# Optimization experiments

Measured on AMD Instinct MI355X. Metric: run time of the kernel, lower is better.

Reference implementation:

```python
import jax, jax.numpy as jnp
import numpy as np

B, LAT, H, N, NL = 16, 64, 128, 256, 3
STATS = 7
IU, JU = np.triu_indices(N, 1)  # P = N*(N-1)/2 upper-triangular pairs


def _ln(x, g, b):
    m = jnp.mean(x, axis=-1, keepdims=True)
    v = jnp.var(x, axis=-1, keepdims=True)
    return (x - m) / jnp.sqrt(v + 1e-5) * g + b


def setup_inputs() -> dict:
    key = jax.random.key(0)
    ks = jax.random.split(key, 16)
    s = 0.02  # xavier-ish small gain per _init_weights
    L = NL - 1
    return {
        "x": jax.random.normal(ks[0], (B, LAT), jnp.float32),
        "stats": jax.random.normal(ks[1], (B, STATS), jnp.float32),
        # input_proj: Linear(LAT+7, 2H) + LN(2H)
        "ip_w": jax.random.normal(ks[2], (LAT + STATS, 2 * H)) * s,
        "ip_b": jnp.zeros((2 * H,)),
        "ip_ln_g": jnp.ones((2 * H,)),
        "ip_ln_b": jnp.zeros((2 * H,)),
        # dim_reduce: Linear(2H, H) + LN(H)
        "dr_w": jax.random.normal(ks[3], (2 * H, H)) * s,
        "dr_b": jnp.zeros((H,)),
        "dr_ln_g": jnp.ones((H,)),
        "dr_ln_b": jnp.zeros((H,)),
        # residual blocks (NL-1 of them), proj is Identity since in==out
        "res_lin1_w": jax.random.normal(ks[4], (L, H, H)) * s,
        "res_lin1_b": jnp.zeros((L, H)),
        "res_lin2_w": jax.random.normal(ks[5], (L, H, H)) * s,
        "res_lin2_b": jnp.zeros((L, H)),
        "res_n1_g": jnp.ones((L, H)),
        "res_n1_b": jnp.zeros((L, H)),
        "res_n2_g": jnp.ones((L, H)),
        "res_n2_b": jnp.zeros((L, H)),
        # attention: Linear(H, 1)
        "attn_w": jax.random.normal(ks[6], (H, 1)) * s,
        "attn_b": jnp.zeros((1,)),
        # edge_mlp: Linear(2H, H) + LN(H) + Linear(H, 2)
        "e1_w": jax.random.normal(ks[7], (2 * H, H)) * s,
        "e1_b": jnp.zeros((H,)),
        "e_ln_g": jnp.ones((H,)),
        "e_ln_b": jnp.zeros((H,)),
        "e2_w": jax.random.normal(ks[8], (H, 2)) * s,
        "e2_b": jnp.zeros((2,)),
        "temperature": jnp.ones((1,)) * 0.5,
    }


def reference(x, stats, ip_w, ip_b, ip_ln_g, ip_ln_b, dr_w, dr_b, dr_ln_g,
              dr_ln_b, res_lin1_w, res_lin1_b, res_lin2_w, res_lin2_b,
              res_n1_g, res_n1_b, res_n2_g, res_n2_b, attn_w, attn_b,
              e1_w, e1_b, e_ln_g, e_ln_b, e2_w, e2_b, temperature):
    # concat latent + stats, broadcast to every node: [B, N, LAT+7]
    z = jnp.concatenate([x, stats], axis=-1)
    z = jnp.broadcast_to(z[:, None, :], (B, N, LAT + STATS))
    # input_proj (dropout is identity in eval)
    h = _ln(jax.nn.relu(z @ ip_w + ip_b), ip_ln_g, ip_ln_b)
    # dim_reduce
    h = _ln(jax.nn.relu(h @ dr_w + dr_b), dr_ln_g, dr_ln_b)
    # residual blocks: h = h + 0.1 * block(h); block(h) = mlp(h) + h
    for l in range(res_lin1_w.shape[0]):
        r = _ln(h, res_n1_g[l], res_n1_b[l])
        r = jax.nn.relu(r @ res_lin1_w[l] + res_lin1_b[l])
        r = _ln(r, res_n2_g[l], res_n2_b[l])
        r = r @ res_lin2_w[l] + res_lin2_b[l]
        h = h + 0.1 * (r + h)
    # simple attention over node axis
    w = jax.nn.softmax(h @ attn_w + attn_b, axis=1)  # [B, N, 1]
    h = h * w
    # batched edge MLP over all i<j pairs: [B, P, 2H]
    edge_in = jnp.concatenate([h[:, IU], h[:, JU]], axis=-1)
    e = _ln(jax.nn.relu(edge_in @ e1_w + e1_b), e_ln_g, e_ln_b)
    logits = e @ e2_w + e2_b  # [B, P, 2]
    # gumbel-softmax (hard, straight-through), fixed key for determinism
    temp = jnp.clip(temperature, 0.1, 2.0)
    u = jax.random.uniform(jax.random.key(42), logits.shape,
                           minval=1e-9, maxval=1.0)
    gumbel = -jnp.log(-jnp.log(u))
    y = jax.nn.softmax((logits + gumbel) / temp, axis=-1)
    y_hard = jax.nn.one_hot(jnp.argmax(y, axis=-1), 2, dtype=y.dtype)
    y = y_hard + y - jax.lax.stop_gradient(y)
    xe = y[..., 0]  # [B, P]
    # scatter into upper triangle, symmetrize
    adj = jnp.zeros((B, N, N), dtype=xe.dtype).at[:, IU, JU].set(xe)
    return adj + jnp.swapaxes(adj, 1, 2)
```

## Files before the change

kernel.cpp:

```cpp
#include <hip/hip_runtime.h>
#include <stdint.h>
#include <math.h>

#define BN 16
#define LATN 64
#define STATSN 7
#define ZN 71
#define HN 128
#define H2N 256
#define NNODE 256
#define NPAIR 32640
#define NQ 522240
#define NT 1024

#define BARRIER() asm volatile("s_waitcnt lgkmcnt(0)\n\ts_barrier" ::: "memory")
#define LGKM0()   asm volatile("s_waitcnt lgkmcnt(0)" ::: "memory")

__device__ __forceinline__ void tf2x32(uint32_t x0, uint32_t x1,
                                       uint32_t& o0, uint32_t& o1) {
    const uint32_t ks0 = 0u, ks1 = 42u, ks2 = 0x1BD11BF0u;
    x0 += ks0; x1 += ks1;
#define TFRND(r) { x0 += x1; x1 = (x1 << (r)) | (x1 >> (32 - (r))); x1 ^= x0; }
    TFRND(13) TFRND(15) TFRND(26) TFRND(6)
    x0 += ks1; x1 += ks2 + 1u;
    TFRND(17) TFRND(29) TFRND(16) TFRND(24)
    x0 += ks2; x1 += ks0 + 2u;
    TFRND(13) TFRND(15) TFRND(26) TFRND(6)
    x0 += ks0; x1 += ks1 + 3u;
    TFRND(17) TFRND(29) TFRND(16) TFRND(24)
    x0 += ks1; x1 += ks2 + 4u;
    TFRND(13) TFRND(15) TFRND(26) TFRND(6)
    x0 += ks2; x1 += ks0 + 5u;
#undef TFRND
    o0 = x0; o1 = x1;
}

__device__ __forceinline__ uint32_t bits_partitionable(uint32_t m) {
    uint32_t o0, o1;
    tf2x32(0u, m, o0, o1);
    return o0 ^ o1;
}

__device__ __forceinline__ float bits_to_u(uint32_t w) {
    float f = __uint_as_float((w >> 9) | 0x3f800000u) - 1.0f;
    const float mn = 1e-9f;
    return fmaxf(mn, f * (1.0f - mn) + mn);
}

template<int CTRL>
__device__ __forceinline__ double dppd(double x) {
    int lo = __double2loint(x), hi = __double2hiint(x);
    lo = __builtin_amdgcn_update_dpp(0, lo, CTRL, 0xF, 0xF, true);
    hi = __builtin_amdgcn_update_dpp(0, hi, CTRL, 0xF, 0xF, true);
    return __hiloint2double(hi, lo);
}
__device__ __forceinline__ double swz16d(double x) {
    int lo = __double2loint(x), hi = __double2hiint(x);
    lo = __builtin_amdgcn_ds_swizzle(lo, 0x401F);
    hi = __builtin_amdgcn_ds_swizzle(hi, 0x401F);
    return __hiloint2double(hi, lo);
}
__device__ __forceinline__ void bfly_pair(double& a, double& q) {
    a += dppd<0xB1>(a);   q += dppd<0xB1>(q);
    a += dppd<0x4E>(a);   q += dppd<0x4E>(q);
    a += dppd<0x141>(a);  q += dppd<0x141>(q);
    a += dppd<0x140>(a);  q += dppd<0x140>(q);
    a += swz16d(a);       q += swz16d(q);
    a += __shfl_xor(a, 32, 64);
    q += __shfl_xor(q, 32, 64);
}

template<int K, int O>
struct WS {
    static constexpr int C    = NT / O;
    static constexpr int KC   = (K + C - 1) / C;
    static constexpr int LOGO = (O == 256) ? 8 : 7;
    float w[KC];
    __device__ __forceinline__ void load(const float* __restrict__ W, int t) {
        const int out = t & (O - 1);
        const int k0 = (t >> LOGO) * KC;
#pragma unroll
        for (int i = 0; i < KC; ++i) {
            const int k = k0 + i;
            w[i] = ((K % C == 0) || k < K) ? W[k * O + out] : 0.0f;
        }
    }
    __device__ __forceinline__ double dot(const double* __restrict__ vin, int t) const {
        const int k0 = (t >> LOGO) * KC;
        double a0 = 0.0, a1 = 0.0;
#pragma unroll
        for (int i = 0; i < KC; i += 2) {
            a0 = fma(vin[k0 + i], (double)w[i], a0);
            if (i + 1 < KC) a1 = fma(vin[k0 + i + 1], (double)w[i + 1], a1);
        }
        return a0 + a1;
    }
    __device__ __forceinline__ double dot_mask127(const double* __restrict__ vin, int t) const {
        const int k0 = (t >> LOGO) * KC;
        double a0 = 0.0, a1 = 0.0;
#pragma unroll
        for (int i = 0; i < KC; i += 2) {
            a0 = fma(vin[(k0 + i) & 127], (double)w[i], a0);
            if (i + 1 < KC) a1 = fma(vin[(k0 + i + 1) & 127], (double)w[i + 1], a1);
        }
        return a0 + a1;
    }
};

template<int NV>
__device__ __forceinline__ void w_stats(const float* v, double& m, double& rs) {
    double a = 0.0, q = 0.0;
#pragma unroll
    for (int i = 0; i < NV; ++i) {
        a += (double)v[i];
        q += (double)v[i] * (double)v[i];
    }
    bfly_pair(a, q);
    constexpr double O = (double)(NV * 64);
    m = a * (1.0 / O);
    const double d = q * (1.0 / O) - m * m + 1e-5;
    double r = (double)rsqrtf((float)d);
    r = r * (1.5 - 0.5 * d * r * r);
    r = r * (1.5 - 0.5 * d * r * r);
    rs = r;
}

#define P_IPB   0
#define P_IPG   256
#define P_IPBB  512
#define P_DRB   768
#define P_DRG   896
#define P_DRBB  1024
#define P_R1B   1152
#define P_N1G   1408
#define P_N1B   1664
#define P_N2G   1920
#define P_N2B   2176
#define P_R2B   2432
#define P_E1B   2688
#define P_EG    2816
#define P_EB    2944
#define P_E2W   3072
#define P_E2B   3328
#define P_SIZE  3332

__global__ __launch_bounds__(NT, 1) void logits_kernel(
    const float* __restrict__ x, const float* __restrict__ st,
    const float* __restrict__ ipw, const float* __restrict__ ipb,
    const float* __restrict__ ipg, const float* __restrict__ ipbb,
    const float* __restrict__ drw, const float* __restrict__ drb,
    const float* __restrict__ drg, const float* __restrict__ drbb,
    const float* __restrict__ r1w, const float* __restrict__ r1b,
    const float* __restrict__ r2w, const float* __restrict__ r2b,
    const float* __restrict__ n1g, const float* __restrict__ n1b,
    const float* __restrict__ n2g, const float* __restrict__ n2b,
    const float* __restrict__ e1w, const float* __restrict__ e1b,
    const float* __restrict__ eg,  const float* __restrict__ eb,
    const float* __restrict__ e2w, const float* __restrict__ e2b,
    float* __restrict__ out_logits)
{
    __shared__ __align__(16) double V0[H2N];
    __shared__ __align__(16) double V1[H2N];
    __shared__ double dpA[NT];
    __shared__ double dpB[NT];
    __shared__ float P[P_SIZE];
    const int t = threadIdx.x;
    const int b = blockIdx.x;
    const int l = t & 63;

    WS<ZN, H2N> w_ip;
    WS<H2N, HN> w_dr;
    WS<HN, HN>  w_r1a, w_r2a, w_r1b, w_r2b;
    WS<H2N, HN> w_e1;

    w_ip.load(ipw, t);
    w_dr.load(drw, t);
    if (t < 256) {
        P[P_IPB + t] = ipb[t];  P[P_IPG + t] = ipg[t];  P[P_IPBB + t] = ipbb[t];
        P[P_R1B + t] = r1b[t];  P[P_N1G + t] = n1g[t];  P[P_N1B + t] = n1b[t];
        P[P_N2G + t] = n2g[t];  P[P_N2B + t] = n2b[t];  P[P_R2B + t] = r2b[t];
        P[P_E2W + t] = e2w[t];
    } else if (t < 384) {
        const int i = t - 256;
        P[P_DRB + i] = drb[i];  P[P_DRG + i] = drg[i];  P[P_DRBB + i] = drbb[i];
        P[P_E1B + i] = e1b[i];  P[P_EG + i] = eg[i];    P[P_EB + i] = eb[i];
    } else if (t < 386) {
        P[P_E2B + (t - 384)] = e2b[t - 384];
    }
    if (t < LATN)      V0[t] = (double)x[b * LATN + t];
    else if (t < ZN)   V0[t] = (double)st[b * STATSN + (t - LATN)];
    else if (t < H2N)  V0[t] = 0.0;
    BARRIER();

    float h0 = 0.0f, h1 = 0.0f;

    dpA[t] = w_ip.dot(V0, t);
    w_r1a.load(r1w, t);
    BARRIER();

    {
        float v[4];
#pragma unroll
        for (int i = 0; i < 4; ++i) {
            const int o = l + 64 * i;
            double ca = 0.0;
#pragma unroll
            for (int cc = 0; cc < 4; ++cc) ca += dpA[o + cc * H2N];
            v[i] = fmaxf((float)ca + P[P_IPB + o], 0.0f);
        }
        double m, rs; w_stats<4>(v, m, rs);
#pragma unroll
        for (int i = 0; i < 4; ++i) {
            const int o = l + 64 * i;
            V1[o] = (double)((float)(((double)v[i] - m) * rs) * P[P_IPG + o] + P[P_IPBB + o]);
        }
    }
    LGKM0();
    dpB[t] = w_dr.dot(V1, t);
    w_r2a.load(r2w, t);
    BARRIER();

    {
        float v[2];
#pragma unroll
        for (int i = 0; i < 2; ++i) {
            const int o = l + 64 * i;
            double ca = 0.0;
#pragma unroll
            for (int cc = 0; cc < 8; ++cc) ca += dpB[o + cc * HN];
            v[i] = fmaxf((float)ca + P[P_DRB + o], 0.0f);
        }
        double m, rs; w_stats<2>(v, m, rs);
        h0 = (float)(((double)v[0] - m) * rs) * P[P_DRG + l] + P[P_DRBB + l];
        h1 = (float)(((double)v[1] - m) * rs) * P[P_DRG + l + 64] + P[P_DRBB + l + 64];
        float hv[2] = {h0, h1};
        double m1, rs1; w_stats<2>(hv, m1, rs1);
        V1[l]      = (double)((float)(((double)h0 - m1) * rs1) * P[P_N1G + l] + P[P_N1B + l]);
        V1[l + 64] = (double)((float)(((double)h1 - m1) * rs1) * P[P_N1G + l + 64] + P[P_N1B + l + 64]);
    }
    LGKM0();
    dpA[t] = w_r1a.dot(V1, t);
    w_r1b.load(r1w + HN * HN, t);
    BARRIER();

    {
        float v[2];
#pragma unroll
        for (int i = 0; i < 2; ++i) {
            const int o = l + 64 * i;
            double ca = 0.0;
#pragma unroll
            for (int cc = 0; cc < 8; ++cc) ca += dpA[o + cc * HN];
            v[i] = fmaxf((float)ca + P[P_R1B + o], 0.0f);
        }
        double m, rs; w_stats<2>(v, m, rs);
        V1[l]      = (double)((float)(((double)v[0] - m) * rs) * P[P_N2G + l] + P[P_N2B + l]);
        V1[l + 64] = (double)((float)(((double)v[1] - m) * rs) * P[P_N2G + l + 64] + P[P_N2B + l + 64]);
    }
    LGKM0();
    dpB[t] = w_r2a.dot(V1, t);
    w_r2b.load(r2w + HN * HN, t);
    BARRIER();

    {
        float r2o[2];
#pragma unroll
        for (int i = 0; i < 2; ++i) {
            const int o = l + 64 * i;
            double ca = 0.0;
#pragma unroll
            for (int cc = 0; cc < 8; ++cc) ca += dpB[o + cc * HN];
            r2o[i] = (float)ca + P[P_R2B + o];
        }
        h0 = h0 + 0.1f * (r2o[0] + h0);
        h1 = h1 + 0.1f * (r2o[1] + h1);
        float hv[2] = {h0, h1};
        double m1, rs1; w_stats<2>(hv, m1, rs1);
        V1[l]      = (double)((float)(((double)h0 - m1) * rs1) * P[P_N1G + HN + l] + P[P_N1B + HN + l]);
        V1[l + 64] = (double)((float)(((double)h1 - m1) * rs1) * P[P_N1G + HN + l + 64] + P[P_N1B + HN + l + 64]);
    }
    LGKM0();
    dpA[t] = w_r1b.dot(V1, t);
    w_e1.load(e1w, t);
    BARRIER();

    {
        float v[2];
#pragma unroll
        for (int i = 0; i < 2; ++i) {
            const int o = l + 64 * i;
            double ca = 0.0;
#pragma unroll
            for (int cc = 0; cc < 8; ++cc) ca += dpA[o + cc * HN];
            v[i] = fmaxf((float)ca + P[P_R1B + HN + o], 0.0f);
        }
        double m, rs; w_stats<2>(v, m, rs);
        V1[l]      = (double)((float)(((double)v[0] - m) * rs) * P[P_N2G + HN + l] + P[P_N2B + HN + l]);
        V1[l + 64] = (double)((float)(((double)v[1] - m) * rs) * P[P_N2G + HN + l + 64] + P[P_N2B + HN + l + 64]);
    }
    LGKM0();
    dpB[t] = w_r2b.dot(V1, t);
    BARRIER();

    {
        float r2o[2];
#pragma unroll
        for (int i = 0; i < 2; ++i) {
            const int o = l + 64 * i;
            double ca = 0.0;
#pragma unroll
            for (int cc = 0; cc < 8; ++cc) ca += dpB[o + cc * HN];
            r2o[i] = (float)ca + P[P_R2B + HN + o];
        }
        h0 = h0 + 0.1f * (r2o[0] + h0);
        h1 = h1 + 0.1f * (r2o[1] + h1);
        V0[l]      = (double)h0;
        V0[l + 64] = (double)h1;
    }
    LGKM0();
    dpA[t] = w_e1.dot_mask127(V0, t) * 0.00390625;
    BARRIER();

    {
        float v[2];
#pragma unroll
        for (int i = 0; i < 2; ++i) {
            const int o = l + 64 * i;
            double ca = 0.0;
#pragma unroll
            for (int cc = 0; cc < 8; ++cc) ca += dpA[o + cc * HN];
            v[i] = fmaxf((float)ca + P[P_E1B + o], 0.0f);
        }
        double m, rs; w_stats<2>(v, m, rs);
        const float eo0 = (float)(((double)v[0] - m) * rs) * P[P_EG + l] + P[P_EB + l];
        const float eo1 = (float)(((double)v[1] - m) * rs) * P[P_EG + l + 64] + P[P_EB + l + 64];
        double p0 = (double)eo0 * (double)P[P_E2W + 2 * l];
        p0 = fma((double)eo1, (double)P[P_E2W + 2 * (l + 64)], p0);
        double p1 = (double)eo0 * (double)P[P_E2W + 2 * l + 1];
        p1 = fma((double)eo1, (double)P[P_E2W + 2 * (l + 64) + 1], p1);
        bfly_pair(p0, p1);
        if (t == 0) {
            out_logits[b * 2]     = (float)p0 + P[P_E2B];
            out_logits[b * 2 + 1] = (float)p1 + P[P_E2B + 1];
        }
    }
}

__device__ __forceinline__ int rowbase(int i) { return (i * (2 * NNODE - 1 - i)) >> 1; }

__global__ __launch_bounds__(256) void edges_kernel(const float* __restrict__ lg,
                                                    const float* __restrict__ tptr,
                                                    float* __restrict__ out)
{
    int q = blockIdx.x * blockDim.x + threadIdx.x;
    if (q >= NQ) return;
    if (q < BN * NNODE) {
        int bb = q >> 8, ii = q & 255;
        out[(bb << 16) | (ii << 8) | ii] = 0.0f;
    }
    float temp = fminf(fmaxf(tptr[0], 0.1f), 2.0f);

    int b = q / NPAIR;
    int p = q - b * NPAIR;
    float discf = 261121.0f - 8.0f * (float)p;
    int i = (int)((511.0f - sqrtf(discf)) * 0.5f);
    if (i < 0) i = 0;
    if (i > NNODE - 2) i = NNODE - 2;
    while (rowbase(i + 1) <= p) ++i;
    while (rowbase(i) > p) --i;
    int j = p - rowbase(i) + i + 1;

    uint32_t w0 = bits_partitionable((uint32_t)(2 * q));
    uint32_t w1 = bits_partitionable((uint32_t)(2 * q + 1));

    float u0 = bits_to_u(w0), u1 = bits_to_u(w1);
    float g0 = -logf(-logf(u0));
    float g1 = -logf(-logf(u1));
    float l0 = lg[2 * b], l1 = lg[2 * b + 1];
    float A0 = (l0 + g0) / temp, A1 = (l1 + g1) / temp;
    float mx = fmaxf(A0, A1);
    float e0 = expf(A0 - mx), e1 = expf(A1 - mx);
    float ssum = e0 + e1;
    float y0 = e0 / ssum, y1 = e1 / ssum;
    float xe = (y0 >= y1) ? 1.0f : 0.0f;
    out[(b << 16) | (i << 8) | j] = xe;
    out[(b << 16) | (j << 8) | i] = xe;
}

extern "C" void kernel_launch(void* const* d_in, const int* in_sizes, int n_in,
                              void* d_out, int out_size, void* d_ws, size_t ws_size,
                              hipStream_t stream)
{
    const float* x    = (const float*)d_in[0];
    const float* st   = (const float*)d_in[1];
    const float* ipw  = (const float*)d_in[2];
    const float* ipb  = (const float*)d_in[3];
    const float* ipg  = (const float*)d_in[4];
    const float* ipbb = (const float*)d_in[5];
    const float* drw  = (const float*)d_in[6];
    const float* drb  = (const float*)d_in[7];
    const float* drg  = (const float*)d_in[8];
    const float* drbb = (const float*)d_in[9];
    const float* r1w  = (const float*)d_in[10];
    const float* r1b  = (const float*)d_in[11];
    const float* r2w  = (const float*)d_in[12];
    const float* r2b  = (const float*)d_in[13];
    const float* n1g  = (const float*)d_in[14];
    const float* n1b  = (const float*)d_in[15];
    const float* n2g  = (const float*)d_in[16];
    const float* n2b  = (const float*)d_in[17];
    const float* e1w  = (const float*)d_in[20];
    const float* e1b  = (const float*)d_in[21];
    const float* eg   = (const float*)d_in[22];
    const float* eb   = (const float*)d_in[23];
    const float* e2w  = (const float*)d_in[24];
    const float* e2b  = (const float*)d_in[25];
    const float* temp = (const float*)d_in[26];
    float* out = (float*)d_out;
    float* lg  = (float*)d_ws;

    hipLaunchKernelGGL(logits_kernel, dim3(BN), dim3(NT), 0, stream,
        x, st, ipw, ipb, ipg, ipbb, drw, drb, drg, drbb,
        r1w, r1b, r2w, r2b, n1g, n1b, n2g, n2b,
        e1w, e1b, eg, eb, e2w, e2b, lg);
    hipLaunchKernelGGL(edges_kernel, dim3((NQ + 255) / 256), dim3(256), 0, stream,
        lg, temp, out);
}
```

Measured before the change: 27.33 us.

## Halve block threads and load weights from global inside each dot product

Reduces the per-batch MLP kernel from 1024 to 512 threads, so each thread covers twice as many K elements per output and the cross-thread partial-sum reduction uses half as many slices. The register-prefetched weight structs are removed, and weights are now read directly from global memory inside each matvec rather than being prefetched one stage ahead. This shrinks register pressure and block size, but exposes global load latency on the serial critical path and lengthens each thread's dot-product chain.

```diff
diff --git a/kernel.cpp b/kernel.cpp
--- a/kernel.cpp
+++ b/kernel.cpp
@@ -11,7 +11,7 @@
 #define NNODE 256
 #define NPAIR 32640
 #define NQ 522240
-#define NT 1024
+#define NT 512
 
 #define BARRIER() asm volatile("s_waitcnt lgkmcnt(0)\n\ts_barrier" ::: "memory")
 #define LGKM0()   asm volatile("s_waitcnt lgkmcnt(0)" ::: "memory")
@@ -70,43 +70,6 @@
     q += __shfl_xor(q, 32, 64);
 }
 
-template<int K, int O>
-struct WS {
-    static constexpr int C    = NT / O;
-    static constexpr int KC   = (K + C - 1) / C;
-    static constexpr int LOGO = (O == 256) ? 8 : 7;
-    float w[KC];
-    __device__ __forceinline__ void load(const float* __restrict__ W, int t) {
-        const int out = t & (O - 1);
-        const int k0 = (t >> LOGO) * KC;
-#pragma unroll
-        for (int i = 0; i < KC; ++i) {
-            const int k = k0 + i;
-            w[i] = ((K % C == 0) || k < K) ? W[k * O + out] : 0.0f;
-        }
-    }
-    __device__ __forceinline__ double dot(const double* __restrict__ vin, int t) const {
-        const int k0 = (t >> LOGO) * KC;
-        double a0 = 0.0, a1 = 0.0;
-#pragma unroll
-        for (int i = 0; i < KC; i += 2) {
-            a0 = fma(vin[k0 + i], (double)w[i], a0);
-            if (i + 1 < KC) a1 = fma(vin[k0 + i + 1], (double)w[i + 1], a1);
-        }
-        return a0 + a1;
-    }
-    __device__ __forceinline__ double dot_mask127(const double* __restrict__ vin, int t) const {
-        const int k0 = (t >> LOGO) * KC;
-        double a0 = 0.0, a1 = 0.0;
-#pragma unroll
-        for (int i = 0; i < KC; i += 2) {
-            a0 = fma(vin[(k0 + i) & 127], (double)w[i], a0);
-            if (i + 1 < KC) a1 = fma(vin[(k0 + i + 1) & 127], (double)w[i + 1], a1);
-        }
-        return a0 + a1;
-    }
-};
-
 template<int NV>
 __device__ __forceinline__ void w_stats(const float* v, double& m, double& rs) {
     double a = 0.0, q = 0.0;
@@ -123,6 +86,34 @@
     r = r * (1.5 - 0.5 * d * r * r);
     r = r * (1.5 - 0.5 * d * r * r);
     rs = r;
+}
+
+template<int K>
+__device__ __forceinline__ double dot128(const float* __restrict__ W,
+                                         const double* __restrict__ vin, int t) {
+    constexpr int KC = K / 4;
+    const int out = t & 127;
+    const int k0 = (t >> 7) * KC;
+    double a0 = 0.0, a1 = 0.0;
+#pragma unroll
+    for (int i = 0; i < KC; i += 2) {
+        a0 = fma(vin[k0 + i], (double)W[(k0 + i) * HN + out], a0);
+        a1 = fma(vin[k0 + i + 1], (double)W[(k0 + i + 1) * HN + out], a1);
+    }
+    return a0 + a1;
+}
+__device__ __forceinline__ double dot128_mask(const float* __restrict__ W,
+                                              const double* __restrict__ vin, int t) {
+    constexpr int KC = 64;
+    const int out = t & 127;
+    const int k0 = (t >> 7) * KC;
+    double a0 = 0.0, a1 = 0.0;
+#pragma unroll
+    for (int i = 0; i < KC; i += 2) {
+        a0 = fma(vin[(k0 + i) & 127], (double)W[(k0 + i) * HN + out], a0);
+        a1 = fma(vin[(k0 + i + 1) & 127], (double)W[(k0 + i + 1) * HN + out], a1);
+    }
+    return a0 + a1;
 }
 
 #define P_IPB   0
@@ -168,13 +159,6 @@
     const int b = blockIdx.x;
     const int l = t & 63;
 
-    WS<ZN, H2N> w_ip;
-    WS<H2N, HN> w_dr;
-    WS<HN, HN>  w_r1a, w_r2a, w_r1b, w_r2b;
-    WS<H2N, HN> w_e1;
-
-    w_ip.load(ipw, t);
-    w_dr.load(drw, t);
     if (t < 256) {
         P[P_IPB + t] = ipb[t];  P[P_IPG + t] = ipg[t];  P[P_IPBB + t] = ipbb[t];
         P[P_R1B + t] = r1b[t];  P[P_N1G + t] = n1g[t];  P[P_N1B + t] = n1b[t];
@@ -189,13 +173,22 @@
     }
     if (t < LATN)      V0[t] = (double)x[b * LATN + t];
     else if (t < ZN)   V0[t] = (double)st[b * STATSN + (t - LATN)];
-    else if (t < H2N)  V0[t] = 0.0;
     BARRIER();
 
     float h0 = 0.0f, h1 = 0.0f;
 
-    dpA[t] = w_ip.dot(V0, t);
-    w_r1a.load(r1w, t);
+    {
+        const int out = t & 255;
+        const int k0 = (t >> 8) * 36;
+        double a0 = 0.0, a1 = 0.0;
+#pragma unroll
+        for (int i = 0; i < 36; i += 2) {
+            const int k = k0 + i;
+            if (k < ZN)     a0 = fma(V0[k], (double)ipw[k * H2N + out], a0);
+            if (k + 1 < ZN) a1 = fma(V0[k + 1], (double)ipw[(k + 1) * H2N + out], a1);
+        }
+        dpA[t] = a0 + a1;
+    }
     BARRIER();
 
     {
@@ -203,9 +196,8 @@
 #pragma unroll
         for (int i = 0; i < 4; ++i) {
             const int o = l + 64 * i;
-            double ca = 0.0;
-#pragma unroll
-            for (int cc = 0; cc < 4; ++cc) ca += dpA[o + cc * H2N];
+            double ca = dpA[o];
+            ca += dpA[o + 256];
             v[i] = fmaxf((float)ca + P[P_IPB + o], 0.0f);
         }
         double m, rs; w_stats<4>(v, m, rs);
@@ -216,8 +208,7 @@
         }
     }
     LGKM0();
-    dpB[t] = w_dr.dot(V1, t);
-    w_r2a.load(r2w, t);
+    dpB[t] = dot128<H2N>(drw, V1, t);
     BARRIER();
 
     {
@@ -227,7 +218,7 @@
             const int o = l + 64 * i;
             double ca = 0.0;
 #pragma unroll
-            for (int cc = 0; cc < 8; ++cc) ca += dpB[o + cc * HN];
+            for (int cc = 0; cc < 4; ++cc) ca += dpB[o + cc * HN];
             v[i] = fmaxf((float)ca + P[P_DRB + o], 0.0f);
         }
         double m, rs; w_stats<2>(v, m, rs);
@@ -239,8 +230,7 @@
         V1[l + 64] = (double)((float)(((double)h1 - m1) * rs1) * P[P_N1G + l + 64] + P[P_N1B + l + 64]);
     }
     LGKM0();
-    dpA[t] = w_r1a.dot(V1, t);
-    w_r1b.load(r1w + HN * HN, t);
+    dpA[t] = dot128<HN>(r1w, V1, t);
     BARRIER();
 
     {
@@ -250,7 +240,7 @@
             const int o = l + 64 * i;
             double ca = 0.0;
 #pragma unroll
-            for (int cc = 0; cc < 8; ++cc) ca += dpA[o + cc * HN];
+            for (int cc = 0; cc < 4; ++cc) ca += dpA[o + cc * HN];
             v[i] = fmaxf((float)ca + P[P_R1B + o], 0.0f);
         }
         double m, rs; w_stats<2>(v, m, rs);
@@ -258,8 +248,7 @@
         V1[l + 64] = (double)((float)(((double)v[1] - m) * rs) * P[P_N2G + l + 64] + P[P_N2B + l + 64]);
     }
     LGKM0();
-    dpB[t] = w_r2a.dot(V1, t);
-    w_r2b.load(r2w + HN * HN, t);
+    dpB[t] = dot128<HN>(r2w, V1, t);
     BARRIER();
 
     {
@@ -269,7 +258,7 @@
             const int o = l + 64 * i;
             double ca = 0.0;
 #pragma unroll
-            for (int cc = 0; cc < 8; ++cc) ca += dpB[o + cc * HN];
+            for (int cc = 0; cc < 4; ++cc) ca += dpB[o + cc * HN];
             r2o[i] = (float)ca + P[P_R2B + o];
         }
         h0 = h0 + 0.1f * (r2o[0] + h0);
@@ -280,8 +269,7 @@
         V1[l + 64] = (double)((float)(((double)h1 - m1) * rs1) * P[P_N1G + HN + l + 64] + P[P_N1B + HN + l + 64]);
     }
     LGKM0();
-    dpA[t] = w_r1b.dot(V1, t);
-    w_e1.load(e1w, t);
+    dpA[t] = dot128<HN>(r1w + HN * HN, V1, t);
     BARRIER();
 
     {
@@ -291,7 +279,7 @@
             const int o = l + 64 * i;
             double ca = 0.0;
 #pragma unroll
-            for (int cc = 0; cc < 8; ++cc) ca += dpA[o + cc * HN];
+            for (int cc = 0; cc < 4; ++cc) ca += dpA[o + cc * HN];
             v[i] = fmaxf((float)ca + P[P_R1B + HN + o], 0.0f);
         }
         double m, rs; w_stats<2>(v, m, rs);
@@ -299,7 +287,7 @@
         V1[l + 64] = (double)((float)(((double)v[1] - m) * rs) * P[P_N2G + HN + l + 64] + P[P_N2B + HN + l + 64]);
     }
     LGKM0();
-    dpB[t] = w_r2b.dot(V1, t);
+    dpB[t] = dot128<HN>(r2w + HN * HN, V1, t);
     BARRIER();
 
     {
@@ -309,7 +297,7 @@
             const int o = l + 64 * i;
             double ca = 0.0;
 #pragma unroll
-            for (int cc = 0; cc < 8; ++cc) ca += dpB[o + cc * HN];
+            for (int cc = 0; cc < 4; ++cc) ca += dpB[o + cc * HN];
             r2o[i] = (float)ca + P[P_R2B + HN + o];
         }
         h0 = h0 + 0.1f * (r2o[0] + h0);
@@ -318,7 +306,7 @@
         V0[l + 64] = (double)h1;
     }
     LGKM0();
-    dpA[t] = w_e1.dot_mask127(V0, t) * 0.00390625;
+    dpA[t] = dot128_mask(e1w, V0, t) * 0.00390625;
     BARRIER();
 
     {
@@ -328,7 +316,7 @@
             const int o = l + 64 * i;
             double ca = 0.0;
 #pragma unroll
-            for (int cc = 0; cc < 8; ++cc) ca += dpA[o + cc * HN];
+            for (int cc = 0; cc < 4; ++cc) ca += dpA[o + cc * HN];
             v[i] = fmaxf((float)ca + P[P_E1B + o], 0.0f);
         }
         double m, rs; w_stats<2>(v, m, rs);
```

After: 28.12 us. 2.9% more time.
